# Performance work log

Hardware: AMD Instinct MI355X
Metric: run time of the kernel (lower is better)

## Reference

```python
import jax, jax.numpy as jnp
import numpy as np

B, H, W, C = 16, 64, 64, 512
NH, WS, SS = 16, 8, 4
HD = C // NH
N = WS * WS
MLP = 4 * C
EPS = 1e-5


def window_partition(x, ws):
    b, h, w, c = x.shape
    x = x.reshape(b, h // ws, ws, w // ws, ws, c).transpose(0, 1, 3, 2, 4, 5)
    return x.reshape(-1, ws, ws, c)


def window_reverse(win, ws, h, w):
    c = win.shape[-1]
    x = win.reshape(-1, h // ws, w // ws, ws, ws, c).transpose(0, 1, 3, 2, 4, 5)
    return x.reshape(-1, h, w, c)


def _rel_pos_index():
    coords = np.stack(np.meshgrid(np.arange(WS), np.arange(WS), indexing='ij'))  # [2,WS,WS]
    cf = coords.reshape(2, -1)
    rc = (cf[:, :, None] - cf[:, None, :]).transpose(1, 2, 0)  # [N,N,2]
    rc[:, :, 0] += WS - 1
    rc[:, :, 1] += WS - 1
    rc[:, :, 0] *= 2 * WS - 1
    return jnp.asarray(rc.sum(-1), dtype=jnp.int32)  # [N,N]


def _attn_mask():
    # region ids for shifted windows (HF get_attn_mask)
    img = np.zeros((1, H, W, 1), dtype=np.float32)
    slices = (slice(0, -WS), slice(-WS, -SS), slice(-SS, None))
    cnt = 0
    for hs in slices:
        for ws_ in slices:
            img[:, hs, ws_, :] = cnt
            cnt += 1
    mw = np.asarray(window_partition(jnp.asarray(img), WS)).reshape(-1, N)  # [nw,N]
    mask = mw[:, None, :] - mw[:, :, None]
    mask = np.where(mask != 0, -100.0, 0.0).astype(np.float32)
    return jnp.asarray(mask)  # [nw,N,N]


REL_IDX = _rel_pos_index()
ATTN_MASK = _attn_mask()


def layer_norm(x, g, b):
    mu = x.mean(-1, keepdims=True)
    var = ((x - mu) ** 2).mean(-1, keepdims=True)
    return (x - mu) * jax.lax.rsqrt(var + EPS) * g + b


def setup_inputs() -> dict:
    key = jax.random.key(0)
    ks = jax.random.split(key, 16)
    s = 0.02
    return {
        'hidden_states': jax.random.normal(ks[0], (B, H * W, C), jnp.float32),
        'q_w': jax.random.normal(ks[1], (C, C), jnp.float32) * s,
        'q_b': jnp.zeros((C,), jnp.float32),
        'k_w': jax.random.normal(ks[2], (C, C), jnp.float32) * s,
        'k_b': jnp.zeros((C,), jnp.float32),
        'v_w': jax.random.normal(ks[3], (C, C), jnp.float32) * s,
        'v_b': jnp.zeros((C,), jnp.float32),
        'proj_w': jax.random.normal(ks[4], (C, C), jnp.float32) * s,
        'proj_b': jnp.zeros((C,), jnp.float32),
        'rel_bias_table': jax.random.normal(ks[5], ((2 * WS - 1) * (2 * WS - 1), NH), jnp.float32) * s,
        'ln1_w': jnp.ones((C,), jnp.float32),
        'ln1_b': jnp.zeros((C,), jnp.float32),
        'ln2_w': jnp.ones((C,), jnp.float32),
        'ln2_b': jnp.zeros((C,), jnp.float32),
        'fc1_w': jax.random.normal(ks[6], (MLP, C), jnp.float32) * s,
        'fc1_b': jnp.zeros((MLP,), jnp.float32),
        'fc2_w': jax.random.normal(ks[7], (C, MLP), jnp.float32) * s,
        'fc2_b': jnp.zeros((C,), jnp.float32),
    }


def reference(hidden_states, q_w, q_b, k_w, k_b, v_w, v_b, proj_w, proj_b,
              rel_bias_table, ln1_w, ln1_b, ln2_w, ln2_b, fc1_w, fc1_b, fc2_w, fc2_b):
    shortcut = hidden_states
    x = layer_norm(hidden_states, ln1_w, ln1_b).reshape(B, H, W, C)
    # cyclic shift
    x = jnp.roll(x, (-SS, -SS), axis=(1, 2))
    win = window_partition(x, WS).reshape(-1, N, C)  # [B*nw, N, C]
    Bw = win.shape[0]

    def heads(t):  # [Bw,N,C] -> [Bw,NH,N,HD]
        return t.reshape(Bw, N, NH, HD).transpose(0, 2, 1, 3)

    q = heads(win @ q_w.T + q_b)
    k = heads(win @ k_w.T + k_b)
    v = heads(win @ v_w.T + v_b)

    scores = jnp.einsum('bhnd,bhmd->bhnm', q, k) / jnp.sqrt(jnp.float32(HD))
    bias = rel_bias_table[REL_IDX.reshape(-1)].reshape(N, N, NH).transpose(2, 0, 1)  # [NH,N,N]
    scores = scores + bias[None]
    nw = ATTN_MASK.shape[0]
    scores = scores.reshape(Bw // nw, nw, NH, N, N) + ATTN_MASK[None, :, None]
    scores = scores.reshape(Bw, NH, N, N)
    probs = jax.nn.softmax(scores, axis=-1)
    ctx = jnp.einsum('bhnm,bhmd->bhnd', probs, v).transpose(0, 2, 1, 3).reshape(Bw, N, C)
    attn_out = ctx @ proj_w.T + proj_b

    shifted = window_reverse(attn_out.reshape(-1, WS, WS, C), WS, H, W)
    x = jnp.roll(shifted, (SS, SS), axis=(1, 2)).reshape(B, H * W, C)
    h = shortcut + x

    y = layer_norm(h, ln2_w, ln2_b)
    y = jax.nn.gelu(y @ fc1_w.T + fc1_b, approximate=False)
    y = y @ fc2_w.T + fc2_b
    return h + y
```

## Files before the change

kernel.cpp:

```cpp
#include <hip/hip_runtime.h>
#include <cmath>
#include <cstdint>
#include <cstddef>

typedef __bf16 bf16;
typedef __bf16 bf16x8 __attribute__((ext_vector_type(8)));
typedef float f32x4 __attribute__((ext_vector_type(4)));

#define DEVINL __device__ __forceinline__

DEVINL void gload_lds16(const bf16* g, bf16* l) {
    __builtin_amdgcn_global_load_lds(
        (const __attribute__((address_space(1))) void*)g,
        (__attribute__((address_space(3))) void*)l,
        16, 0, 0);
}

DEVINL bool probe_f32(const uint32_t* probe) { return *probe == 0x3F800000u; }

#define OFF_QW  0u
#define OFF_KW  262144u
#define OFF_VW  524288u
#define OFF_PW  786432u
#define OFF_F1W 1048576u
#define OFF_F2W 2097152u
#define OFF_REL 3145728u
#define OFF_QB  3149328u
#define OFF_KB  3149840u
#define OFF_VB  3150352u
#define OFF_PB  3150864u
#define OFF_L1W 3151376u
#define OFF_L1B 3151888u
#define OFF_L2W 3152400u
#define OFF_L2B 3152912u
#define OFF_F1B 3153424u
#define OFF_F2B 3155472u
#define PRM_TOT 3155984u

struct P17 { const void* p[17]; };

__global__ __launch_bounds__(256) void conv_params(P17 ps, const uint32_t* probe,
                                                   bf16* __restrict__ dst) {
    const size_t off[18] = {OFF_QW, OFF_KW, OFF_VW, OFF_PW, OFF_F1W, OFF_F2W,
                            OFF_REL, OFF_QB, OFF_KB, OFF_VB, OFF_PB, OFF_L1W,
                            OFF_L1B, OFF_L2W, OFF_L2B, OFF_F1B, OFF_F2B, PRM_TOT};
    size_t e = ((size_t)blockIdx.x * 256 + threadIdx.x) * 8;
    if (e >= PRM_TOT) return;
    int s = 0;
#pragma unroll
    for (int i = 1; i < 17; ++i) s = (e >= off[i]) ? i : s;
    const size_t loc = e - off[s];
    if (probe_f32(probe)) {
        const float* sp = (const float*)ps.p[s] + loc;
        bf16x8 o;
#pragma unroll
        for (int t = 0; t < 8; ++t) o[t] = (bf16)sp[t];
        *(bf16x8*)(dst + e) = o;
    } else {
        *(bf16x8*)(dst + e) = *(const bf16x8*)((const bf16*)ps.p[s] + loc);
    }
}

__global__ __launch_bounds__(256) void conv_hidden(const void* __restrict__ src,
                                                   const uint32_t* probe,
                                                   bf16* __restrict__ dst,
                                                   size_t base_elt) {
    size_t e = ((size_t)blockIdx.x * 256 + threadIdx.x) * 8;
    if (probe_f32(probe)) {
        const float* sp = (const float*)src + base_elt + e;
        bf16x8 o;
#pragma unroll
        for (int t = 0; t < 8; ++t) o[t] = (bf16)sp[t];
        *(bf16x8*)(dst + e) = o;
    } else {
        *(bf16x8*)(dst + e) = *(const bf16x8*)((const bf16*)src + base_elt + e);
    }
}

template <int MODE>
__global__ __launch_bounds__(256) void ln_kernel(const bf16* __restrict__ srcb,
                                                 const float* __restrict__ srcf,
                                                 const bf16* __restrict__ g,
                                                 const bf16* __restrict__ bb,
                                                 bf16* __restrict__ out) {
    const int row = blockIdx.x * 4 + (threadIdx.x >> 6);
    const int lane = threadIdx.x & 63;
    size_t srow;
    if (MODE == 0) {
        int win = row >> 6, t = row & 63;
        int b = win >> 6, wi = win & 63;
        int hs = ((wi >> 3) << 3) + (t >> 3);
        int ws = ((wi & 7) << 3) + (t & 7);
        srow = (size_t)b * 4096 + (size_t)((hs + 4) & 63) * 64 + ((ws + 4) & 63);
    } else {
        srow = row;
    }
    float x[8];
    if (MODE == 0) {
        bf16x8 vv = *(const bf16x8*)(srcb + srow * 512 + lane * 8);
#pragma unroll
        for (int t = 0; t < 8; ++t) x[t] = (float)vv[t];
    } else {
        const f32x4* p = (const f32x4*)(srcf + srow * 512 + lane * 8);
        f32x4 a = p[0], c = p[1];
#pragma unroll
        for (int t = 0; t < 4; ++t) { x[t] = a[t]; x[4 + t] = c[t]; }
    }
    float s = 0.f, s2 = 0.f;
#pragma unroll
    for (int t = 0; t < 8; ++t) { s += x[t]; s2 += x[t] * x[t]; }
    for (int off = 1; off < 64; off <<= 1) {
        s += __shfl_xor(s, off, 64);
        s2 += __shfl_xor(s2, off, 64);
    }
    const float mu = s * (1.0f / 512.0f);
    const float var = s2 * (1.0f / 512.0f) - mu * mu;
    const float rs = rsqrtf(var + 1e-5f);
    bf16x8 gg = *(const bf16x8*)(g + lane * 8);
    bf16x8 bv = *(const bf16x8*)(bb + lane * 8);
    bf16x8 o;
#pragma unroll
    for (int t = 0; t < 8; ++t)
        o[t] = (bf16)(((x[t] - mu) * rs) * (float)gg[t] + (float)bv[t]);
    *(bf16x8*)(out + (size_t)row * 512 + lane * 8) = o;
}

template <int N, int K, int EPI>
__global__ __launch_bounds__(256) void gemm_bt(const bf16* __restrict__ A,
                                               const bf16* __restrict__ W,
                                               const bf16* __restrict__ bias,
                                               void* __restrict__ outp,
                                               const bf16* __restrict__ auxb,
                                               const float* __restrict__ auxf,
                                               size_t obase,
                                               const uint32_t* probe) {
    static_assert(K % 64 == 0, "K must be a multiple of 64");
    __shared__ __align__(16) char sA[16384];
    __shared__ __align__(16) char sB[16384];
    const int tid = threadIdx.x;
    const int bm = blockIdx.x, bn = blockIdx.y;
    const int wave = tid >> 6, lane = tid & 63;
    const int wm = (wave >> 1) << 6, wn = (wave & 1) << 6;
    const int lrow = lane & 15, quad = lane >> 4;

    const uint32_t rsw = (uint32_t)(lrow & 7) << 4;
    const uint32_t cb0 = ((uint32_t)(quad * 16)) ^ rsw;
    const uint32_t cb1 = ((uint32_t)(quad * 16 + 64)) ^ rsw;
    const int sswz = (tid & 56) << 1;
    const uint32_t arow = (uint32_t)(wm + lrow) * 128u;
    const uint32_t brow = (uint32_t)(wn + lrow) * 128u;

    bool f32o = false;
    if constexpr (EPI == 3) f32o = probe_f32(probe);

    f32x4 acc[4][4] = {};
    const bf16* Ab = A + (size_t)bm * 128 * K;
    const bf16* Wb = W + (size_t)bn * 128 * K;

    for (int k0 = 0; k0 < K; k0 += 64) {
#pragma unroll
        for (int r = 0; r < 4; ++r) {
            const int X = r * 4096 + tid * 16;
            const int sx = X ^ sswz;
            const int row = sx >> 7, col = (sx & 127) >> 1;
            gload_lds16(Ab + (size_t)row * K + k0 + col, (bf16*)(sA + X));
            gload_lds16(Wb + (size_t)row * K + k0 + col, (bf16*)(sB + X));
        }
        __syncthreads();
        bf16x8 af[4][2], bfr[4][2];
#pragma unroll
        for (int i = 0; i < 4; ++i) {
            af[i][0]  = *(const bf16x8*)(sA + (arow + i * 2048 + cb0));
            af[i][1]  = *(const bf16x8*)(sA + (arow + i * 2048 + cb1));
            bfr[i][0] = *(const bf16x8*)(sB + (brow + i * 2048 + cb0));
            bfr[i][1] = *(const bf16x8*)(sB + (brow + i * 2048 + cb1));
        }
#pragma unroll
        for (int i = 0; i < 4; ++i)
#pragma unroll
            for (int j = 0; j < 4; ++j)
#pragma unroll
                for (int ks = 0; ks < 2; ++ks)
                    acc[i][j] = __builtin_amdgcn_mfma_f32_16x16x32_bf16(
                        af[i][ks], bfr[j][ks], acc[i][j], 0, 0, 0);
        __syncthreads();
    }

#pragma unroll
    for (int i = 0; i < 4; ++i) {
#pragma unroll
        for (int r = 0; r < 4; ++r) {
            const int m = bm * 128 + wm + i * 16 + quad * 4 + r;
            size_t dest = 0;
            if (EPI == 1) {
                int win = m >> 6, t = m & 63;
                int b = win >> 6, wi = win & 63;
                int hs = ((wi >> 3) << 3) + (t >> 3);
                int ws = ((wi & 7) << 3) + (t & 7);
                dest = (size_t)b * 4096 + (size_t)((hs + 4) & 63) * 64 + ((ws + 4) & 63);
            }
#pragma unroll
            for (int j = 0; j < 4; ++j) {
                const int n = bn * 128 + wn + j * 16 + lrow;
                float v = acc[i][j][r] + (float)bias[n];
                if (EPI == 0) {
                    ((bf16*)outp)[(size_t)m * N + n] = (bf16)v;
                } else if (EPI == 1) {
                    ((float*)outp)[dest * 512 + n] = v + (float)auxb[dest * 512 + n];
                } else if (EPI == 2) {
                    float gl = 0.5f * v * (1.0f + erff(v * 0.70710678118654752f));
                    ((bf16*)outp)[(size_t)m * N + n] = (bf16)gl;
                } else {
                    float o = v + auxf[(size_t)m * N + n];
                    if (f32o) ((float*)outp)[obase + (size_t)m * N + n] = o;
                    else      ((bf16*)outp)[obase + (size_t)m * N + n] = (bf16)o;
                }
            }
        }
    }
}

__global__ __launch_bounds__(256) void attn_kernel(const bf16* __restrict__ q,
                                                   const bf16* __restrict__ k,
                                                   const bf16* __restrict__ v,
                                                   const bf16* __restrict__ table,
                                                   bf16* __restrict__ ctx) {
    __shared__ bf16 sVt[4][32 * 64];
    __shared__ bf16 sP[4][64 * 64];
    const int win = blockIdx.x;
    const int wave = threadIdx.x >> 6, lane = threadIdx.x & 63;
    const int head = blockIdx.y * 4 + wave;
    const int lrow = lane & 15, quad = lane >> 4;
    const size_t base = (size_t)win * 64 * 512 + head * 32;

    {
        const bf16* vr = v + base + (size_t)lane * 512;
#pragma unroll
        for (int d0 = 0; d0 < 32; d0 += 8) {
            bf16x8 vv = *(const bf16x8*)(vr + d0);
#pragma unroll
            for (int t = 0; t < 8; ++t) sVt[wave][(d0 + t) * 64 + lane] = vv[t];
        }
    }

    f32x4 sacc[4][4] = {};
    {
        bf16x8 qa[4], kb[4];
#pragma unroll
        for (int i = 0; i < 4; ++i)
            qa[i] = *(const bf16x8*)(q + base + (size_t)(i * 16 + lrow) * 512 + quad * 8);
#pragma unroll
        for (int j = 0; j < 4; ++j)
            kb[j] = *(const bf16x8*)(k + base + (size_t)(j * 16 + lrow) * 512 + quad * 8);
#pragma unroll
        for (int i = 0; i < 4; ++i)
#pragma unroll
            for (int j = 0; j < 4; ++j)
                sacc[i][j] = __builtin_amdgcn_mfma_f32_16x16x32_bf16(qa[i], kb[j], sacc[i][j], 0, 0, 0);
    }

    const int wi = win & 63;
    const int hb8 = (wi >> 3) << 3, wb8 = (wi & 7) << 3;
    const float scale = 0.17677669529663689f;
#pragma unroll
    for (int ti = 0; ti < 4; ++ti) {
#pragma unroll
        for (int r = 0; r < 4; ++r) {
            const int i = ti * 16 + quad * 4 + r;
            const int ih = i >> 3, iw = i & 7;
            const int ah = hb8 + ih, aw = wb8 + iw;
            const int rgi = ((ah < 56) ? 0 : (ah < 60) ? 1 : 2) * 3 +
                            ((aw < 56) ? 0 : (aw < 60) ? 1 : 2);
            float rowmax = -1e30f;
#pragma unroll
            for (int tj = 0; tj < 4; ++tj) {
                const int j = tj * 16 + lrow;
                const int jh = j >> 3, jw = j & 7;
                const int bh = hb8 + jh, bw = wb8 + jw;
                const int rgj = ((bh < 56) ? 0 : (bh < 60) ? 1 : 2) * 3 +
                                ((bw < 56) ? 0 : (bw < 60) ? 1 : 2);
                const int ridx = (ih - jh + 7) * 15 + (iw - jw + 7);
                float sv = sacc[ti][tj][r] * scale + (float)table[ridx * 16 + head] +
                           ((rgi == rgj) ? 0.0f : -100.0f);
                sacc[ti][tj][r] = sv;
                rowmax = fmaxf(rowmax, sv);
            }
            for (int off = 1; off < 16; off <<= 1)
                rowmax = fmaxf(rowmax, __shfl_xor(rowmax, off, 64));
            float rsum = 0.f;
#pragma unroll
            for (int tj = 0; tj < 4; ++tj) {
                float e = __expf(sacc[ti][tj][r] - rowmax);
                sacc[ti][tj][r] = e;
                rsum += e;
            }
            for (int off = 1; off < 16; off <<= 1) rsum += __shfl_xor(rsum, off, 64);
            const float inv = 1.0f / rsum;
#pragma unroll
            for (int tj = 0; tj < 4; ++tj)
                sP[wave][(size_t)i * 64 + tj * 16 + lrow] = (bf16)(sacc[ti][tj][r] * inv);
        }
    }
    __syncthreads();

    f32x4 cacc[4][2] = {};
#pragma unroll
    for (int ks = 0; ks < 2; ++ks) {
        bf16x8 vbf[2];
#pragma unroll
        for (int tn = 0; tn < 2; ++tn)
            vbf[tn] = *(const bf16x8*)&sVt[wave][(tn * 16 + lrow) * 64 + ks * 32 + quad * 8];
#pragma unroll
        for (int mi = 0; mi < 4; ++mi) {
            bf16x8 pa = *(const bf16x8*)&sP[wave][(size_t)(mi * 16 + lrow) * 64 + ks * 32 + quad * 8];
#pragma unroll
            for (int tn = 0; tn < 2; ++tn)
                cacc[mi][tn] = __builtin_amdgcn_mfma_f32_16x16x32_bf16(pa, vbf[tn], cacc[mi][tn], 0, 0, 0);
        }
    }
#pragma unroll
    for (int mi = 0; mi < 4; ++mi)
#pragma unroll
        for (int tn = 0; tn < 2; ++tn)
#pragma unroll
            for (int r = 0; r < 4; ++r) {
                const int i = mi * 16 + quad * 4 + r;
                const int d = tn * 16 + lrow;
                ctx[base + (size_t)i * 512 + d] = (bf16)cacc[mi][tn][r];
            }
}

extern "C" void kernel_launch(void* const* d_in, const int* in_sizes, int n_in,
                              void* d_out, int out_size, void* d_ws, size_t ws_size,
                              hipStream_t stream) {
    (void)in_sizes; (void)n_in; (void)out_size;
    const uint32_t* probe = (const uint32_t*)d_in[10];
    char* ws = (char*)d_ws;
    const size_t MB = (size_t)1 << 20;

    bf16* prm = (bf16*)ws;
    P17 ps;
    ps.p[0] = d_in[1];  ps.p[1] = d_in[3];  ps.p[2] = d_in[5];  ps.p[3] = d_in[7];
    ps.p[4] = d_in[14]; ps.p[5] = d_in[16]; ps.p[6] = d_in[9];  ps.p[7] = d_in[2];
    ps.p[8] = d_in[4];  ps.p[9] = d_in[6];  ps.p[10] = d_in[8]; ps.p[11] = d_in[10];
    ps.p[12] = d_in[11]; ps.p[13] = d_in[12]; ps.p[14] = d_in[13];
    ps.p[15] = d_in[15]; ps.p[16] = d_in[17];
    conv_params<<<dim3((PRM_TOT / 8 + 255) / 256), dim3(256), 0, stream>>>(ps, probe, prm);

    int nb = 1;
    for (int c = 16; c >= 2; c >>= 1)
        if (8 * MB + (size_t)c * 36 * MB <= ws_size) { nb = c; break; }
    const size_t R = (size_t)nb * 4096;
    char* arena = ws + 8 * MB;
    bf16* hidC = (bf16*)(arena);
    bf16* Xc   = (bf16*)(arena + 1024 * R);
    bf16* qc   = (bf16*)(arena + 2048 * R);
    bf16* kc   = (bf16*)(arena + 3072 * R);
    bf16* vc   = (bf16*)(arena + 4096 * R);
    float* hc  = (float*)(arena + 5120 * R);
    bf16* a1   = (bf16*)(arena + 7168 * R);

    const int nchunks = 16 / nb;
    const size_t Mh = R / 2;

    for (int cb = 0; cb < nchunks; ++cb) {
        conv_hidden<<<dim3((unsigned)(R / 4)), dim3(256), 0, stream>>>(
            d_in[0], probe, hidC, (size_t)cb * R * 512);

        ln_kernel<0><<<dim3((unsigned)(R / 4)), dim3(256), 0, stream>>>(
            hidC, nullptr, prm + OFF_L1W, prm + OFF_L1B, Xc);

        gemm_bt<512, 512, 0><<<dim3((unsigned)(R / 128), 4), dim3(256), 0, stream>>>(
            Xc, prm + OFF_QW, prm + OFF_QB, qc, nullptr, nullptr, 0, nullptr);
        gemm_bt<512, 512, 0><<<dim3((unsigned)(R / 128), 4), dim3(256), 0, stream>>>(
            Xc, prm + OFF_KW, prm + OFF_KB, kc, nullptr, nullptr, 0, nullptr);
        gemm_bt<512, 512, 0><<<dim3((unsigned)(R / 128), 4), dim3(256), 0, stream>>>(
            Xc, prm + OFF_VW, prm + OFF_VB, vc, nullptr, nullptr, 0, nullptr);

        attn_kernel<<<dim3((unsigned)(R / 64), 4), dim3(256), 0, stream>>>(
            qc, kc, vc, prm + OFF_REL, Xc);

        gemm_bt<512, 512, 1><<<dim3((unsigned)(R / 128), 4), dim3(256), 0, stream>>>(
            Xc, prm + OFF_PW, prm + OFF_PB, hc, hidC, nullptr, 0, nullptr);

        ln_kernel<1><<<dim3((unsigned)(R / 4)), dim3(256), 0, stream>>>(
            nullptr, hc, prm + OFF_L2W, prm + OFF_L2B, Xc);

        for (int hf = 0; hf < 2; ++hf) {
            gemm_bt<2048, 512, 2><<<dim3((unsigned)(Mh / 128), 16), dim3(256), 0, stream>>>(
                Xc + (size_t)hf * Mh * 512, prm + OFF_F1W, prm + OFF_F1B, a1,
                nullptr, nullptr, 0, nullptr);
            gemm_bt<512, 2048, 3><<<dim3((unsigned)(Mh / 128), 4), dim3(256), 0, stream>>>(
                a1, prm + OFF_F2W, prm + OFF_F2B, d_out,
                nullptr, hc + (size_t)hf * Mh * 512,
                ((size_t)cb * R + (size_t)hf * Mh) * 512, probe);
        }
    }
}
```

Baseline: 1.222 ms.

## Fuse QKV projections, fold input conversion into LayerNorm, swizzle GEMM block order

The three separate Q/K/V GEMMs become one N=1536 GEMM, relying on the q/k/v weights and biases sitting contiguously in the param buffer. Attention reads from the interleaved qkv buffer with a 1536 stride. The hidden-state conversion kernel is folded into the first LayerNorm, which also writes the bf16 shortcut copy. GEMMs now use a 1D grid with an XCD-style block-index swizzle to improve L2 locality across chiplets. The risks are divisibility assumptions in the swizzle (grid size must be a multiple of 8) and strided attention loads.

```diff
diff --git a/kernel.cpp b/kernel.cpp
--- a/kernel.cpp
+++ b/kernel.cpp
@@ -61,28 +61,15 @@
     }
 }
 
-__global__ __launch_bounds__(256) void conv_hidden(const void* __restrict__ src,
-                                                   const uint32_t* probe,
-                                                   bf16* __restrict__ dst,
-                                                   size_t base_elt) {
-    size_t e = ((size_t)blockIdx.x * 256 + threadIdx.x) * 8;
-    if (probe_f32(probe)) {
-        const float* sp = (const float*)src + base_elt + e;
-        bf16x8 o;
-#pragma unroll
-        for (int t = 0; t < 8; ++t) o[t] = (bf16)sp[t];
-        *(bf16x8*)(dst + e) = o;
-    } else {
-        *(bf16x8*)(dst + e) = *(const bf16x8*)((const bf16*)src + base_elt + e);
-    }
-}
-
 template <int MODE>
-__global__ __launch_bounds__(256) void ln_kernel(const bf16* __restrict__ srcb,
+__global__ __launch_bounds__(256) void ln_kernel(const void* __restrict__ src0,
+                                                 const uint32_t* __restrict__ probe,
                                                  const float* __restrict__ srcf,
                                                  const bf16* __restrict__ g,
                                                  const bf16* __restrict__ bb,
-                                                 bf16* __restrict__ out) {
+                                                 bf16* __restrict__ out,
+                                                 bf16* __restrict__ hidC,
+                                                 size_t base_elt) {
     const int row = blockIdx.x * 4 + (threadIdx.x >> 6);
     const int lane = threadIdx.x & 63;
     size_t srow;
@@ -97,9 +84,21 @@
     }
     float x[8];
     if (MODE == 0) {
-        bf16x8 vv = *(const bf16x8*)(srcb + srow * 512 + lane * 8);
-#pragma unroll
-        for (int t = 0; t < 8; ++t) x[t] = (float)vv[t];
+        bf16x8 cv;
+        if (probe_f32(probe)) {
+            const float* sp = (const float*)src0 + base_elt + srow * 512 + lane * 8;
+            const f32x4* p = (const f32x4*)sp;
+            f32x4 a = p[0], c = p[1];
+#pragma unroll
+            for (int t = 0; t < 4; ++t) { x[t] = a[t]; x[4 + t] = c[t]; }
+#pragma unroll
+            for (int t = 0; t < 8; ++t) cv[t] = (bf16)x[t];
+        } else {
+            cv = *(const bf16x8*)((const bf16*)src0 + base_elt + srow * 512 + lane * 8);
+#pragma unroll
+            for (int t = 0; t < 8; ++t) x[t] = (float)cv[t];
+        }
+        *(bf16x8*)(hidC + srow * 512 + lane * 8) = cv;
     } else {
         const f32x4* p = (const f32x4*)(srcf + srow * 512 + lane * 8);
         f32x4 a = p[0], c = p[1];
@@ -135,10 +134,16 @@
                                                size_t obase,
                                                const uint32_t* probe) {
     static_assert(K % 64 == 0, "K must be a multiple of 64");
+    static_assert(N % 128 == 0, "N must be a multiple of 128");
     __shared__ __align__(16) char sA[16384];
     __shared__ __align__(16) char sB[16384];
     const int tid = threadIdx.x;
-    const int bm = blockIdx.x, bn = blockIdx.y;
+    constexpr int NBN = N / 128;
+    const int nwg = (int)gridDim.x;
+    const int bid = (int)blockIdx.x;
+    const int swz = (bid & 7) * (nwg >> 3) + (bid >> 3);
+    const int bm = swz / NBN, bn = swz % NBN;
+
     const int wave = tid >> 6, lane = tid & 63;
     const int wm = (wave >> 1) << 6, wn = (wave & 1) << 6;
     const int lrow = lane & 15, quad = lane >> 4;
@@ -220,9 +225,7 @@
     }
 }
 
-__global__ __launch_bounds__(256) void attn_kernel(const bf16* __restrict__ q,
-                                                   const bf16* __restrict__ k,
-                                                   const bf16* __restrict__ v,
+__global__ __launch_bounds__(256) void attn_kernel(const bf16* __restrict__ qkv,
                                                    const bf16* __restrict__ table,
                                                    bf16* __restrict__ ctx) {
     __shared__ bf16 sVt[4][32 * 64];
@@ -231,10 +234,11 @@
     const int wave = threadIdx.x >> 6, lane = threadIdx.x & 63;
     const int head = blockIdx.y * 4 + wave;
     const int lrow = lane & 15, quad = lane >> 4;
-    const size_t base = (size_t)win * 64 * 512 + head * 32;
+    const size_t baseq = (size_t)win * 64 * 1536 + head * 32;
+    const size_t basec = (size_t)win * 64 * 512 + head * 32;
 
     {
-        const bf16* vr = v + base + (size_t)lane * 512;
+        const bf16* vr = qkv + baseq + 1024 + (size_t)lane * 1536;
 #pragma unroll
         for (int d0 = 0; d0 < 32; d0 += 8) {
             bf16x8 vv = *(const bf16x8*)(vr + d0);
@@ -248,10 +252,10 @@
         bf16x8 qa[4], kb[4];
 #pragma unroll
         for (int i = 0; i < 4; ++i)
-            qa[i] = *(const bf16x8*)(q + base + (size_t)(i * 16 + lrow) * 512 + quad * 8);
+            qa[i] = *(const bf16x8*)(qkv + baseq + (size_t)(i * 16 + lrow) * 1536 + quad * 8);
 #pragma unroll
         for (int j = 0; j < 4; ++j)
-            kb[j] = *(const bf16x8*)(k + base + (size_t)(j * 16 + lrow) * 512 + quad * 8);
+            kb[j] = *(const bf16x8*)(qkv + baseq + 512 + (size_t)(j * 16 + lrow) * 1536 + quad * 8);
 #pragma unroll
         for (int i = 0; i < 4; ++i)
 #pragma unroll
@@ -326,7 +330,7 @@
             for (int r = 0; r < 4; ++r) {
                 const int i = mi * 16 + quad * 4 + r;
                 const int d = tn * 16 + lrow;
-                ctx[base + (size_t)i * 512 + d] = (bf16)cacc[mi][tn][r];
+                ctx[basec + (size_t)i * 512 + d] = (bf16)cacc[mi][tn][r];
             }
 }
 
@@ -354,9 +358,7 @@
     char* arena = ws + 8 * MB;
     bf16* hidC = (bf16*)(arena);
     bf16* Xc   = (bf16*)(arena + 1024 * R);
-    bf16* qc   = (bf16*)(arena + 2048 * R);
-    bf16* kc   = (bf16*)(arena + 3072 * R);
-    bf16* vc   = (bf16*)(arena + 4096 * R);
+    bf16* qkv  = (bf16*)(arena + 2048 * R);
     float* hc  = (float*)(arena + 5120 * R);
     bf16* a1   = (bf16*)(arena + 7168 * R);
 
@@ -364,33 +366,27 @@
     const size_t Mh = R / 2;
 
     for (int cb = 0; cb < nchunks; ++cb) {
-        conv_hidden<<<dim3((unsigned)(R / 4)), dim3(256), 0, stream>>>(
-            d_in[0], probe, hidC, (size_t)cb * R * 512);
-
         ln_kernel<0><<<dim3((unsigned)(R / 4)), dim3(256), 0, stream>>>(
-            hidC, nullptr, prm + OFF_L1W, prm + OFF_L1B, Xc);
-
-        gemm_bt<512, 512, 0><<<dim3((unsigned)(R / 128), 4), dim3(256), 0, stream>>>(
-            Xc, prm + OFF_QW, prm + OFF_QB, qc, nullptr, nullptr, 0, nullptr);
-        gemm_bt<512, 512, 0><<<dim3((unsigned)(R / 128), 4), dim3(256), 0, stream>>>(
-            Xc, prm + OFF_KW, prm + OFF_KB, kc, nullptr, nullptr, 0, nullptr);
-        gemm_bt<512, 512, 0><<<dim3((unsigned)(R / 128), 4), dim3(256), 0, stream>>>(
-            Xc, prm + OFF_VW, prm + OFF_VB, vc, nullptr, nullptr, 0, nullptr);
+            d_in[0], probe, nullptr, prm + OFF_L1W, prm + OFF_L1B, Xc, hidC,
+            (size_t)cb * R * 512);
+
+        gemm_bt<1536, 512, 0><<<dim3((unsigned)(R / 128) * 12), dim3(256), 0, stream>>>(
+            Xc, prm + OFF_QW, prm + OFF_QB, qkv, nullptr, nullptr, 0, nullptr);
 
         attn_kernel<<<dim3((unsigned)(R / 64), 4), dim3(256), 0, stream>>>(
-            qc, kc, vc, prm + OFF_REL, Xc);
-
-        gemm_bt<512, 512, 1><<<dim3((unsigned)(R / 128), 4), dim3(256), 0, stream>>>(
+            qkv, prm + OFF_REL, Xc);
+
+        gemm_bt<512, 512, 1><<<dim3((unsigned)(R / 128) * 4), dim3(256), 0, stream>>>(
             Xc, prm + OFF_PW, prm + OFF_PB, hc, hidC, nullptr, 0, nullptr);
 
         ln_kernel<1><<<dim3((unsigned)(R / 4)), dim3(256), 0, stream>>>(
-            nullptr, hc, prm + OFF_L2W, prm + OFF_L2B, Xc);
+            nullptr, nullptr, hc, prm + OFF_L2W, prm + OFF_L2B, Xc, nullptr, 0);
 
         for (int hf = 0; hf < 2; ++hf) {
-            gemm_bt<2048, 512, 2><<<dim3((unsigned)(Mh / 128), 16), dim3(256), 0, stream>>>(
+            gemm_bt<2048, 512, 2><<<dim3((unsigned)(Mh / 128) * 16), dim3(256), 0, stream>>>(
                 Xc + (size_t)hf * Mh * 512, prm + OFF_F1W, prm + OFF_F1B, a1,
                 nullptr, nullptr, 0, nullptr);
-            gemm_bt<512, 2048, 3><<<dim3((unsigned)(Mh / 128), 4), dim3(256), 0, stream>>>(
+            gemm_bt<512, 2048, 3><<<dim3((unsigned)(Mh / 128) * 4), dim3(256), 0, stream>>>(
                 a1, prm + OFF_F2W, prm + OFF_F2B, d_out,
                 nullptr, hc + (size_t)hf * Mh * 512,
                 ((size_t)cb * R + (size_t)hf * Mh) * 512, probe);
```

New measurement: 1.181 ms. 3.3% less time.
